# Kernel optimization log

Measured on AMD Instinct MI355X. Metric: run time of the kernel, lower is better.

Reference implementation:

```python
import jax, jax.numpy as jnp
import numpy as np

D_MODEL = 1024
SCALE = float(np.sqrt(D_MODEL))


def setup_inputs() -> dict:
    key = jax.random.key(0)
    k1, k2, k3 = jax.random.split(key, 3)
    input_data = jax.random.normal(k1, (4, 2048, D_MODEL), dtype=jnp.float32)
    qk = jax.random.normal(k2, (D_MODEL, D_MODEL), dtype=jnp.float32) / SCALE
    ov = jax.random.normal(k3, (D_MODEL, D_MODEL), dtype=jnp.float32) / SCALE
    return {"input_data": input_data, "qk": qk, "ov": ov}


def reference(input_data, qk, ov):
    # input_data: [B, S, D]; qk, ov: [D, D]
    S = input_data.shape[1]
    # scores: [B, S, S] = (x @ qk) @ x^T / sqrt(D)
    scores = jnp.einsum("bsd,de,bte->bst", input_data, qk, input_data) / SCALE
    # causal mask: positions t > s get -inf (upper triangle, diagonal=1)
    causal = jnp.tril(jnp.ones((S, S), dtype=bool))
    scores = jnp.where(causal, scores, -jnp.inf)
    attn = jax.nn.softmax(scores, axis=-1)
    # A: [B, S, D] = attn @ x @ ov
    return jnp.einsum("bst,btd,de->bse", attn, input_data, ov)
```

## Files before the change

### kernel.cpp

```cpp
#include <hip/hip_runtime.h>
#include <hip/hip_bf16.h>
#include <cstdint>
#include <cstddef>
#include <type_traits>


using bf16 = __hip_bfloat16;
typedef __attribute__((ext_vector_type(8))) short short8;
typedef __attribute__((ext_vector_type(4))) float f32x4;

#define NB 4
#define SS 2048
#define DD 1024

__device__ __forceinline__ void async_lds16(const bf16* g, bf16* l) {
  __builtin_amdgcn_global_load_lds(
      (const __attribute__((address_space(1))) void*)g,
      (__attribute__((address_space(3))) void*)l,
      16, 0, 0);
}

struct alignas(8) bf16x4s { bf16 a, b, c, d; };

__global__ __launch_bounds__(256) void prep_kernel(const float* __restrict__ x,
                                                   bf16* __restrict__ xb,
                                                   const float* __restrict__ qk,
                                                   bf16* __restrict__ qkT,
                                                   const float* __restrict__ ov,
                                                   bf16* __restrict__ ovT,
                                                   float* __restrict__ l) {
  __shared__ bf16 tile[64][65];
  const int bx = blockIdx.x;
  if (bx < 8192) {
    int i = (bx * 256 + threadIdx.x) * 4;
    float4 v = *(const float4*)(x + i);
    bf16x4s o{__float2bfloat16(v.x), __float2bfloat16(v.y),
              __float2bfloat16(v.z), __float2bfloat16(v.w)};
    *(bf16x4s*)(xb + i) = o;
  } else if (bx < 8704) {
    const int idx = bx - 8192;
    const float* in = (idx & 256) ? ov : qk;
    bf16* out = (idx & 256) ? ovT : qkT;
    const int rem = idx & 255;
    const int tbx = (rem & 15) * 64;
    const int tby = (rem >> 4) * 64;
    const int tc = threadIdx.x & 63;
    const int tr = threadIdx.x >> 6;
#pragma unroll
    for (int r = tr; r < 64; r += 4)
      tile[tc][r] = __float2bfloat16(in[(size_t)(tby + r) * DD + tbx + tc]);
    __syncthreads();
#pragma unroll
    for (int r = tr; r < 64; r += 4)
      out[(size_t)(tbx + r) * DD + tby + tc] = tile[r][tc];
  } else {
    const int t = (bx - 8704) * 256 + threadIdx.x;
    f32x4 z = {0.f, 0.f, 0.f, 0.f};
    *(f32x4*)(l + t * 4) = z;
  }
}

__device__ __forceinline__ void gemm256_core(const bf16* __restrict__ Ab,
                                             const bf16* __restrict__ Bb,
                                             bf16* __restrict__ C,
                                             int N, int K, int m0, int n0, int nk,
                                             bf16* As, bf16* Bs) {
  const int lane = threadIdx.x & 63;
  const int wave = threadIdx.x >> 6;
  const int wr   = wave >> 2;
  const int wc   = wave & 3;
  const int quad = lane >> 4;
  const int r    = lane & 15;

  f32x4 acc[8][4];
#pragma unroll
  for (int i = 0; i < 8; ++i)
#pragma unroll
    for (int n = 0; n < 4; ++n) acc[i][n] = f32x4{0.f, 0.f, 0.f, 0.f};

  const int lrow = lane >> 3;
  const int lsw  = (lane & 7) ^ lrow;
  const long long a_lane = (long long)(m0 + wave * 8 + lrow) * K + lsw * 8;
  const long long b_lane = (long long)(n0 + wave * 8 + lrow) * K + lsw * 8;

  auto stageA = [&](int kt, int rnd, int buf) {
    async_lds16(Ab + a_lane + (long long)(rnd * 64) * K + (long long)kt * 64,
                As + buf * 16384 + (rnd * 64 + wave * 8) * 64);
  };
  auto stageB = [&](int kt, int rnd, int buf) {
    async_lds16(Bb + b_lane + (long long)(rnd * 64) * K + (long long)kt * 64,
                Bs + buf * 16384 + (rnd * 64 + wave * 8) * 64);
  };

  stageA(0, 0, 0); stageA(0, 2, 0);
  stageB(0, 0, 0); stageB(0, 1, 0); stageB(0, 2, 0); stageB(0, 3, 0);
  stageA(0, 1, 0); stageA(0, 3, 0);
  asm volatile("s_waitcnt vmcnt(2)" ::: "memory");
  asm volatile("s_barrier" ::: "memory");

  const int ca0 = (quad ^ (r & 7)) * 8;
  const int ca1 = ((4 + quad) ^ (r & 7)) * 8;

  for (int kt = 0; kt < nk; ++kt) {
    const int buf = kt & 1, nxt = buf ^ 1;
    const bool hn = (kt + 1 < nk);
    const bf16* Abuf = As + buf * 16384 + (wr * 128) * 64;
    const bf16* Bbuf = Bs + buf * 16384 + (wc * 64) * 64;

    auto phase = [&](auto RHC, int ca, auto&& stg, int wmode) {
      constexpr int RH = decltype(RHC)::value;
      short8 af[4], bfr[4];
#pragma unroll
      for (int m = 0; m < 4; ++m)
        af[m] = *(const short8*)(Abuf + (RH * 64 + m * 16 + r) * 64 + ca);
#pragma unroll
      for (int n = 0; n < 4; ++n)
        bfr[n] = *(const short8*)(Bbuf + (n * 16 + r) * 64 + ca);
      stg();
      asm volatile("s_barrier" ::: "memory");
      asm volatile("s_waitcnt lgkmcnt(0)" ::: "memory");
      __builtin_amdgcn_sched_barrier(0);
      __builtin_amdgcn_s_setprio(1);
#pragma unroll
      for (int m = 0; m < 4; ++m)
#pragma unroll
        for (int n = 0; n < 4; ++n)
          acc[RH * 4 + m][n] = __builtin_amdgcn_mfma_f32_16x16x32_bf16(
              af[m], bfr[n], acc[RH * 4 + m][n], 0, 0, 0);
      __builtin_amdgcn_s_setprio(0);
      if (wmode == 1) {
        if (hn) asm volatile("s_waitcnt vmcnt(2)" ::: "memory");
        else    asm volatile("s_waitcnt vmcnt(0)" ::: "memory");
      } else if (wmode == 2) {
        if (hn) asm volatile("s_waitcnt vmcnt(2)" ::: "memory");
      }
      asm volatile("s_barrier" ::: "memory");
    };

    phase(std::integral_constant<int, 0>{}, ca0,
          [&] { if (hn) { stageA(kt + 1, 0, nxt); stageA(kt + 1, 2, nxt); } }, 1);
    phase(std::integral_constant<int, 1>{}, ca0,
          [&] { if (hn) { stageB(kt + 1, 0, nxt); stageB(kt + 1, 1, nxt); } }, 0);
    phase(std::integral_constant<int, 0>{}, ca1,
          [&] { if (hn) { stageB(kt + 1, 2, nxt); stageB(kt + 1, 3, nxt); } }, 0);
    phase(std::integral_constant<int, 1>{}, ca1,
          [&] { if (hn) { stageA(kt + 1, 1, nxt); stageA(kt + 1, 3, nxt); } }, 2);
  }

#pragma unroll
  for (int i = 0; i < 8; ++i) {
    const int row0 = m0 + wr * 128 + i * 16 + quad * 4;
#pragma unroll
    for (int n = 0; n < 4; ++n) {
      const int col = n0 + wc * 64 + n * 16 + r;
#pragma unroll
      for (int q = 0; q < 4; ++q)
        C[(long long)(row0 + q) * N + col] = __float2bfloat16(acc[i][n][q]);
    }
  }
}

template <int EPI>
__device__ __forceinline__ void gemm128_core(const bf16* __restrict__ Ab,
                                             const bf16* __restrict__ Bb,
                                             void* __restrict__ C,
                                             float* __restrict__ l,
                                             int N, int K, int m0, int n0, int nk,
                                             bf16* As, bf16* Bs) {
  const int lane = threadIdx.x & 63;
  const int wave = threadIdx.x >> 6;
  const int wr   = wave >> 1;
  const int wc   = wave & 1;
  const int quad = lane >> 4;
  const int r    = lane & 15;

  f32x4 acc[4][4];
#pragma unroll
  for (int m = 0; m < 4; ++m)
#pragma unroll
    for (int n = 0; n < 4; ++n) acc[m][n] = f32x4{0.f, 0.f, 0.f, 0.f};

  const int lrow = lane >> 3;
  const int lsw  = (lane & 7) ^ lrow;
  const long long a_base = (long long)(m0 + wave * 32 + lrow) * K + lsw * 8;
  const long long b_base = (long long)(n0 + wave * 32 + lrow) * K + lsw * 8;

  auto stageA = [&](int kt, int buf) {
#pragma unroll
    for (int i = 0; i < 4; ++i)
      async_lds16(Ab + a_base + (long long)(i * 8) * K + (long long)kt * 64,
                  As + buf * 8192 + (wave * 32 + i * 8) * 64);
  };
  auto stageB = [&](int kt, int buf) {
#pragma unroll
    for (int i = 0; i < 4; ++i)
      async_lds16(Bb + b_base + (long long)(i * 8) * K + (long long)kt * 64,
                  Bs + buf * 8192 + (wave * 32 + i * 8) * 64);
  };

  stageB(0, 0); stageA(0, 0); stageA(1, 1);
  asm volatile("s_waitcnt vmcnt(4)" ::: "memory");
  asm volatile("s_barrier" ::: "memory");

  const int ca0 = (quad ^ (r & 7)) * 8;
  const int ca1 = ((4 + quad) ^ (r & 7)) * 8;

  int ba = 0;
  for (int kt = 0; kt < nk; ++kt) {
    const int bb = kt & 1;
    int ba2 = ba + 2; if (ba2 >= 3) ba2 -= 3;
    const bool hA = (kt + 2 < nk), hB = (kt + 1 < nk);
    const bf16* Abuf = As + ba * 8192;
    const bf16* Bbuf = Bs + bb * 8192;

    auto phase = [&](int ca, auto&& stg, bool tail) {
      short8 af[4], bfr[4];
#pragma unroll
      for (int m = 0; m < 4; ++m)
        af[m] = *(const short8*)(Abuf + (wr * 64 + m * 16 + r) * 64 + ca);
#pragma unroll
      for (int n = 0; n < 4; ++n)
        bfr[n] = *(const short8*)(Bbuf + (wc * 64 + n * 16 + r) * 64 + ca);
      stg();
      asm volatile("s_barrier" ::: "memory");
      asm volatile("s_waitcnt lgkmcnt(0)" ::: "memory");
      __builtin_amdgcn_sched_barrier(0);
      __builtin_amdgcn_s_setprio(1);
#pragma unroll
      for (int m = 0; m < 4; ++m)
#pragma unroll
        for (int n = 0; n < 4; ++n)
          acc[m][n] = __builtin_amdgcn_mfma_f32_16x16x32_bf16(
              af[m], bfr[n], acc[m][n], 0, 0, 0);
      __builtin_amdgcn_s_setprio(0);
      if (tail) {
        if (hA)      asm volatile("s_waitcnt vmcnt(4)" ::: "memory");
        else if (hB) asm volatile("s_waitcnt vmcnt(0)" ::: "memory");
      }
      asm volatile("s_barrier" ::: "memory");
    };

    phase(ca0, [&] { if (hB) stageB(kt + 1, bb ^ 1);
                     if (hA) stageA(kt + 2, ba2); }, false);
    phase(ca1, [&] {}, true);

    if (++ba == 3) ba = 0;
  }

#pragma unroll
  for (int m = 0; m < 4; ++m) {
    const int row0 = m0 + wr * 64 + m * 16 + quad * 4;
    if (EPI == 2) {
      float qs[4] = {0.f, 0.f, 0.f, 0.f};
#pragma unroll
      for (int n = 0; n < 4; ++n) {
        const int col = n0 + wc * 64 + n * 16 + r;
#pragma unroll
        for (int q = 0; q < 4; ++q) {
          const int row = row0 + q;
          float v = (col <= row) ? __expf(acc[m][n][q] * 0.03125f) : 0.0f;
          ((bf16*)C)[(long long)row * N + col] = __float2bfloat16(v);
          qs[q] += v;
        }
      }
#pragma unroll
      for (int q = 0; q < 4; ++q) {
#pragma unroll
        for (int off = 1; off < 16; off <<= 1) qs[q] += __shfl_xor(qs[q], off, 64);
        if (r == 0) atomicAdd(&l[row0 + q], qs[q]);
      }
    } else {
      float rs[4];
#pragma unroll
      for (int q = 0; q < 4; ++q) rs[q] = 1.0f / l[row0 + q];
#pragma unroll
      for (int n = 0; n < 4; ++n) {
        const int col = n0 + wc * 64 + n * 16 + r;
#pragma unroll
        for (int q = 0; q < 4; ++q)
          ((float*)C)[(long long)(row0 + q) * N + col] = acc[m][n][q] * rs[q];
      }
    }
  }
}

__global__ __launch_bounds__(512, 2) void gemm_qv256(const bf16* __restrict__ xb,
                                                     const bf16* __restrict__ qkT,
                                                     const bf16* __restrict__ ovT,
                                                     bf16* __restrict__ Qb,
                                                     bf16* __restrict__ Vt) {
  extern __shared__ bf16 lds[];
  bf16* As = lds;
  bf16* Bs = lds + 32768;
  const long long SD = (long long)SS * DD;
  const int z = blockIdx.z;
  if (z < 4) {
    const int bn = blockIdx.x & 3, bm = blockIdx.x >> 2;
    gemm256_core(xb + z * SD, qkT, Qb + z * SD, DD, DD, bm * 256, bn * 256, 16, As, Bs);
  } else {
    const int bm = blockIdx.x & 3, bn = blockIdx.x >> 2;
    gemm256_core(ovT, xb + (z - 4) * SD, Vt + (z - 4) * SD, SS, DD, bm * 256, bn * 256, 16, As, Bs);
  }
}

__global__ __launch_bounds__(256, 2) void gemm_sc128(const bf16* __restrict__ Qb,
                                                     const bf16* __restrict__ xb,
                                                     bf16* __restrict__ P,
                                                     float* __restrict__ l) {
  extern __shared__ bf16 lds[];
  bf16* As = lds;
  bf16* Bs = lds + 24576;
  const long long SD = (long long)SS * DD;
  const long long SSQ = (long long)SS * SS;
  const int t = blockIdx.x;
  int bm = (int)((sqrtf(8.0f * (float)t + 1.0f) - 1.0f) * 0.5f);
  while ((bm + 1) * (bm + 2) / 2 <= t) ++bm;
  while (bm * (bm + 1) / 2 > t) --bm;
  const int bn = t - bm * (bm + 1) / 2;
  const int b = blockIdx.z;
  gemm128_core<2>(Qb + b * SD, xb + b * SD, P + b * SSQ, l + b * SS,
                  SS, DD, bm * 128, bn * 128, 16, As, Bs);
}

__global__ __launch_bounds__(256, 2) void gemm_pv128(const bf16* __restrict__ P,
                                                     const bf16* __restrict__ Vt,
                                                     float* __restrict__ l,
                                                     float* __restrict__ out) {
  extern __shared__ bf16 lds[];
  bf16* As = lds;
  bf16* Bs = lds + 24576;
  const long long SD = (long long)SS * DD;
  const long long SSQ = (long long)SS * SS;
  const int c  = blockIdx.x & 7;
  const int pr = blockIdx.x >> 3;
  const int b  = blockIdx.z;
  const int n0 = c * 128;
  const int rL = 15 - pr;
  gemm128_core<3>(P + b * SSQ, Vt + b * SD, out + b * SD, l + b * SS,
                  DD, SS, rL * 128, n0, 2 * (rL + 1), As, Bs);
  __syncthreads();
  gemm128_core<3>(P + b * SSQ, Vt + b * SD, out + b * SD, l + b * SS,
                  DD, SS, pr * 128, n0, 2 * (pr + 1), As, Bs);
}

extern "C" void kernel_launch(void* const* d_in, const int* in_sizes, int n_in,
                              void* d_out, int out_size, void* d_ws, size_t ws_size,
                              hipStream_t stream) {
  const float* x  = (const float*)d_in[0];
  const float* qk = (const float*)d_in[1];
  const float* ov = (const float*)d_in[2];
  float* out = (float*)d_out;

  char* ws = (char*)d_ws;
  const size_t MB = 1ull << 20;
  bf16*  xb  = (bf16*)(ws + 0);
  bf16*  qkT = (bf16*)(ws + 16 * MB);
  bf16*  ovT = (bf16*)(ws + 18 * MB);
  bf16*  Qb  = (bf16*)(ws + 20 * MB);
  bf16*  Vt  = (bf16*)(ws + 36 * MB);
  bf16*  P   = (bf16*)(ws + 52 * MB);
  float* l   = (float*)(ws + 84 * MB);

  static bool lds_opt_in = false;
  if (!lds_opt_in) {
    hipFuncSetAttribute((const void*)gemm_qv256,
                        hipFuncAttributeMaxDynamicSharedMemorySize, 131072);
    hipFuncSetAttribute((const void*)gemm_sc128,
                        hipFuncAttributeMaxDynamicSharedMemorySize, 81920);
    hipFuncSetAttribute((const void*)gemm_pv128,
                        hipFuncAttributeMaxDynamicSharedMemorySize, 81920);
    lds_opt_in = true;
  }

  prep_kernel<<<dim3(8712), 256, 0, stream>>>(x, xb, qk, qkT, ov, ovT, l);
  gemm_qv256<<<dim3(32, 1, 8), 512, 131072, stream>>>(xb, qkT, ovT, Qb, Vt);
  gemm_sc128<<<dim3(136, 1, 4), 256, 81920, stream>>>(Qb, xb, P, l);
  gemm_pv128<<<dim3(64, 1, 4), 256, 81920, stream>>>(P, Vt, l, out);
}
```

Baseline: 199.0 us.

## Use BK=32 K-tiles with a 4-stage unified LDS pipeline in gemm128_core

The 128x128 GEMM core goes from 64-wide K tiles (3 A buffers, 2 B buffers, two half-phases per tile) to 32-wide K tiles held in a 4-deep ring shared by A and B, prefetching three tiles ahead. The swizzle, load mapping and waitcnt accounting are rewritten to match, and the dynamic LDS request drops from 80KB to 64KB. The intent is deeper memory latency hiding and a simpler schedule with less LDS. In exchange each iteration does half the MFMA work per barrier pair, so sync overhead per FLOP roughly doubles.

New measurement: 201.4 us. Within noise of the previous version (+1.2%).

```diff
diff --git a/kernel.cpp b/kernel.cpp
--- a/kernel.cpp
+++ b/kernel.cpp
@@ -180,71 +180,65 @@
 #pragma unroll
     for (int n = 0; n < 4; ++n) acc[m][n] = f32x4{0.f, 0.f, 0.f, 0.f};
 
-  const int lrow = lane >> 3;
-  const int lsw  = (lane & 7) ^ lrow;
+  const int lrow = lane >> 2;
+  const int lsw  = (lane & 3) ^ (lrow & 3);
   const long long a_base = (long long)(m0 + wave * 32 + lrow) * K + lsw * 8;
   const long long b_base = (long long)(n0 + wave * 32 + lrow) * K + lsw * 8;
 
   auto stageA = [&](int kt, int buf) {
 #pragma unroll
-    for (int i = 0; i < 4; ++i)
-      async_lds16(Ab + a_base + (long long)(i * 8) * K + (long long)kt * 64,
-                  As + buf * 8192 + (wave * 32 + i * 8) * 64);
+    for (int i = 0; i < 2; ++i)
+      async_lds16(Ab + a_base + (long long)(i * 16) * K + (long long)kt * 32,
+                  As + buf * 4096 + (wave * 32 + i * 16) * 32);
   };
   auto stageB = [&](int kt, int buf) {
 #pragma unroll
-    for (int i = 0; i < 4; ++i)
-      async_lds16(Bb + b_base + (long long)(i * 8) * K + (long long)kt * 64,
-                  Bs + buf * 8192 + (wave * 32 + i * 8) * 64);
+    for (int i = 0; i < 2; ++i)
+      async_lds16(Bb + b_base + (long long)(i * 16) * K + (long long)kt * 32,
+                  Bs + buf * 4096 + (wave * 32 + i * 16) * 32);
   };
 
-  stageB(0, 0); stageA(0, 0); stageA(1, 1);
-  asm volatile("s_waitcnt vmcnt(4)" ::: "memory");
+  stageB(0, 0); stageA(0, 0);
+  if (nk > 1) { stageB(1, 1); stageA(1, 1); }
+  if (nk > 2) { stageB(2, 2); stageA(2, 2); }
+  if (nk > 2)      asm volatile("s_waitcnt vmcnt(8)" ::: "memory");
+  else if (nk > 1) asm volatile("s_waitcnt vmcnt(4)" ::: "memory");
+  else             asm volatile("s_waitcnt vmcnt(0)" ::: "memory");
   asm volatile("s_barrier" ::: "memory");
 
-  const int ca0 = (quad ^ (r & 7)) * 8;
-  const int ca1 = ((4 + quad) ^ (r & 7)) * 8;
-
-  int ba = 0;
-  for (int kt = 0; kt < nk; ++kt) {
-    const int bb = kt & 1;
-    int ba2 = ba + 2; if (ba2 >= 3) ba2 -= 3;
-    const bool hA = (kt + 2 < nk), hB = (kt + 1 < nk);
-    const bf16* Abuf = As + ba * 8192;
-    const bf16* Bbuf = Bs + bb * 8192;
-
-    auto phase = [&](int ca, auto&& stg, bool tail) {
-      short8 af[4], bfr[4];
-#pragma unroll
-      for (int m = 0; m < 4; ++m)
-        af[m] = *(const short8*)(Abuf + (wr * 64 + m * 16 + r) * 64 + ca);
+  const int ca = (quad ^ (r & 3)) * 8;
+
+  for (int t = 0; t < nk; ++t) {
+    const int bt = t & 3, b3 = (t + 3) & 3;
+    const bf16* Abuf = As + bt * 4096;
+    const bf16* Bbuf = Bs + bt * 4096;
+
+    short8 af[4], bfr[4];
+#pragma unroll
+    for (int m = 0; m < 4; ++m)
+      af[m] = *(const short8*)(Abuf + (wr * 64 + m * 16 + r) * 32 + ca);
+#pragma unroll
+    for (int n = 0; n < 4; ++n)
+      bfr[n] = *(const short8*)(Bbuf + (wc * 64 + n * 16 + r) * 32 + ca);
+
+    if (t + 3 < nk) { stageB(t + 3, b3); stageA(t + 3, b3); }
+
+    asm volatile("s_barrier" ::: "memory");
+    asm volatile("s_waitcnt lgkmcnt(0)" ::: "memory");
+    __builtin_amdgcn_sched_barrier(0);
+    __builtin_amdgcn_s_setprio(1);
+#pragma unroll
+    for (int m = 0; m < 4; ++m)
 #pragma unroll
       for (int n = 0; n < 4; ++n)
-        bfr[n] = *(const short8*)(Bbuf + (wc * 64 + n * 16 + r) * 64 + ca);
-      stg();
-      asm volatile("s_barrier" ::: "memory");
-      asm volatile("s_waitcnt lgkmcnt(0)" ::: "memory");
-      __builtin_amdgcn_sched_barrier(0);
-      __builtin_amdgcn_s_setprio(1);
-#pragma unroll
-      for (int m = 0; m < 4; ++m)
-#pragma unroll
-        for (int n = 0; n < 4; ++n)
-          acc[m][n] = __builtin_amdgcn_mfma_f32_16x16x32_bf16(
-              af[m], bfr[n], acc[m][n], 0, 0, 0);
-      __builtin_amdgcn_s_setprio(0);
-      if (tail) {
-        if (hA)      asm volatile("s_waitcnt vmcnt(4)" ::: "memory");
-        else if (hB) asm volatile("s_waitcnt vmcnt(0)" ::: "memory");
-      }
-      asm volatile("s_barrier" ::: "memory");
-    };
-
-    phase(ca0, [&] { if (hB) stageB(kt + 1, bb ^ 1);
-                     if (hA) stageA(kt + 2, ba2); }, false);
-    phase(ca1, [&] {}, true);
-
-    if (++ba == 3) ba = 0;
+        acc[m][n] = __builtin_amdgcn_mfma_f32_16x16x32_bf16(
+            af[m], bfr[n], acc[m][n], 0, 0, 0);
+    __builtin_amdgcn_s_setprio(0);
+
+    if (t + 3 < nk)      asm volatile("s_waitcnt vmcnt(8)" ::: "memory");
+    else if (t + 2 < nk) asm volatile("s_waitcnt vmcnt(4)" ::: "memory");
+    else if (t + 1 < nk) asm volatile("s_waitcnt vmcnt(0)" ::: "memory");
+    asm volatile("s_barrier" ::: "memory");
   }
 
 #pragma unroll
@@ -309,7 +303,7 @@
                                                      float* __restrict__ l) {
   extern __shared__ bf16 lds[];
   bf16* As = lds;
-  bf16* Bs = lds + 24576;
+  bf16* Bs = lds + 16384;
   const long long SD = (long long)SS * DD;
   const long long SSQ = (long long)SS * SS;
   const int t = blockIdx.x;
@@ -319,7 +313,7 @@
   const int bn = t - bm * (bm + 1) / 2;
   const int b = blockIdx.z;
   gemm128_core<2>(Qb + b * SD, xb + b * SD, P + b * SSQ, l + b * SS,
-                  SS, DD, bm * 128, bn * 128, 16, As, Bs);
+                  SS, DD, bm * 128, bn * 128, 32, As, Bs);
 }
 
 __global__ __launch_bounds__(256, 2) void gemm_pv128(const bf16* __restrict__ P,
@@ -328,7 +322,7 @@
                                                      float* __restrict__ out) {
   extern __shared__ bf16 lds[];
   bf16* As = lds;
-  bf16* Bs = lds + 24576;
+  bf16* Bs = lds + 16384;
   const long long SD = (long long)SS * DD;
   const long long SSQ = (long long)SS * SS;
   const int c  = blockIdx.x & 7;
@@ -337,10 +331,10 @@
   const int n0 = c * 128;
   const int rL = 15 - pr;
   gemm128_core<3>(P + b * SSQ, Vt + b * SD, out + b * SD, l + b * SS,
-                  DD, SS, rL * 128, n0, 2 * (rL + 1), As, Bs);
+                  DD, SS, rL * 128, n0, 4 * (rL + 1), As, Bs);
   __syncthreads();
   gemm128_core<3>(P + b * SSQ, Vt + b * SD, out + b * SD, l + b * SS,
-                  DD, SS, pr * 128, n0, 2 * (pr + 1), As, Bs);
+                  DD, SS, pr * 128, n0, 4 * (pr + 1), As, Bs);
 }
 
 extern "C" void kernel_launch(void* const* d_in, const int* in_sizes, int n_in,
@@ -366,14 +360,14 @@
     hipFuncSetAttribute((const void*)gemm_qv256,
                         hipFuncAttributeMaxDynamicSharedMemorySize, 131072);
     hipFuncSetAttribute((const void*)gemm_sc128,
-                        hipFuncAttributeMaxDynamicSharedMemorySize, 81920);
+                        hipFuncAttributeMaxDynamicSharedMemorySize, 65536);
     hipFuncSetAttribute((const void*)gemm_pv128,
-                        hipFuncAttributeMaxDynamicSharedMemorySize, 81920);
+                        hipFuncAttributeMaxDynamicSharedMemorySize, 65536);
     lds_opt_in = true;
   }
 
   prep_kernel<<<dim3(8712), 256, 0, stream>>>(x, xb, qk, qkT, ov, ovT, l);
   gemm_qv256<<<dim3(32, 1, 8), 512, 131072, stream>>>(xb, qkT, ovT, Qb, Vt);
-  gemm_sc128<<<dim3(136, 1, 4), 256, 81920, stream>>>(Qb, xb, P, l);
-  gemm_pv128<<<dim3(64, 1, 4), 256, 81920, stream>>>(P, Vt, l, out);
-}
+  gemm_sc128<<<dim3(136, 1, 4), 256, 65536, stream>>>(Qb, xb, P, l);
+  gemm_pv128<<<dim3(64, 1, 4), 256, 65536, stream>>>(P, Vt, l, out);
+}
```

## Use 64x128 tiles for causal score GEMM with finer triangular block mapping

Applied to the files above, without the earlier changes.

Replaces the 128x128 score GEMM with a dedicated 64x128 tile kernel that uses double-buffered LDS, a smaller LDS footprint and three blocks per CU. A new block-index mapping enumerates 64-row strips against 128-column tiles of the causal triangle, so fewer fully masked tiles are computed and more blocks are available to fill the GPU. In exchange each block reuses less data from its loads, and the pipeline is simpler than the original three-stage A buffering.

After: 191.8 us, median of 3. -3.6%, faster.

```diff
diff --git a/kernel.cpp b/kernel.cpp
--- a/kernel.cpp
+++ b/kernel.cpp
@@ -160,13 +160,113 @@
   }
 }
 
-template <int EPI>
-__device__ __forceinline__ void gemm128_core(const bf16* __restrict__ Ab,
-                                             const bf16* __restrict__ Bb,
-                                             void* __restrict__ C,
-                                             float* __restrict__ l,
-                                             int N, int K, int m0, int n0, int nk,
-                                             bf16* As, bf16* Bs) {
+__device__ __forceinline__ void gemm64_sc(const bf16* __restrict__ Ab,
+                                          const bf16* __restrict__ Bb,
+                                          bf16* __restrict__ P,
+                                          float* __restrict__ l,
+                                          int N, int K, int m0, int n0, int nk,
+                                          bf16* As, bf16* Bs) {
+  const int lane = threadIdx.x & 63;
+  const int wave = threadIdx.x >> 6;
+  const int wm   = (wave >> 1) * 32;
+  const int wn   = (wave & 1) * 64;
+  const int quad = lane >> 4;
+  const int r    = lane & 15;
+
+  f32x4 acc[2][4];
+#pragma unroll
+  for (int m = 0; m < 2; ++m)
+#pragma unroll
+    for (int n = 0; n < 4; ++n) acc[m][n] = f32x4{0.f, 0.f, 0.f, 0.f};
+
+  const int lrow = lane >> 3;
+  const int lsw  = (lane & 7) ^ lrow;
+  const long long a_lane = (long long)(m0 + lrow) * K + lsw * 8;
+  const long long b_lane = (long long)(n0 + lrow) * K + lsw * 8;
+
+  auto stageA = [&](int kt, int rnd, int buf) {
+    async_lds16(Ab + a_lane + (long long)(rnd * 32 + wave * 8) * K + (long long)kt * 64,
+                As + buf * 4096 + (rnd * 32 + wave * 8) * 64);
+  };
+  auto stageB = [&](int kt, int rnd, int buf) {
+    async_lds16(Bb + b_lane + (long long)(rnd * 32 + wave * 8) * K + (long long)kt * 64,
+                Bs + buf * 8192 + (rnd * 32 + wave * 8) * 64);
+  };
+
+  stageA(0, 0, 0); stageA(0, 1, 0);
+  stageB(0, 0, 0); stageB(0, 1, 0); stageB(0, 2, 0); stageB(0, 3, 0);
+  asm volatile("s_waitcnt vmcnt(0)" ::: "memory");
+  asm volatile("s_barrier" ::: "memory");
+
+  const int ca0 = (quad ^ (r & 7)) * 8;
+  const int ca1 = ((4 + quad) ^ (r & 7)) * 8;
+
+  for (int kt = 0; kt < nk; ++kt) {
+    const int buf = kt & 1, nxt = buf ^ 1;
+    const bool hn = (kt + 1 < nk);
+    const bf16* Abuf = As + buf * 4096;
+    const bf16* Bbuf = Bs + buf * 8192;
+
+    auto phase = [&](int ca, auto&& stg, bool tail) {
+      short8 af[2], bfr[4];
+#pragma unroll
+      for (int m = 0; m < 2; ++m)
+        af[m] = *(const short8*)(Abuf + (wm + m * 16 + r) * 64 + ca);
+#pragma unroll
+      for (int n = 0; n < 4; ++n)
+        bfr[n] = *(const short8*)(Bbuf + (wn + n * 16 + r) * 64 + ca);
+      stg();
+      asm volatile("s_barrier" ::: "memory");
+      asm volatile("s_waitcnt lgkmcnt(0)" ::: "memory");
+      __builtin_amdgcn_sched_barrier(0);
+      __builtin_amdgcn_s_setprio(1);
+#pragma unroll
+      for (int m = 0; m < 2; ++m)
+#pragma unroll
+        for (int n = 0; n < 4; ++n)
+          acc[m][n] = __builtin_amdgcn_mfma_f32_16x16x32_bf16(
+              af[m], bfr[n], acc[m][n], 0, 0, 0);
+      __builtin_amdgcn_s_setprio(0);
+      if (tail && hn) asm volatile("s_waitcnt vmcnt(0)" ::: "memory");
+      asm volatile("s_barrier" ::: "memory");
+    };
+
+    phase(ca0, [&] { if (hn) { stageA(kt + 1, 0, nxt); stageA(kt + 1, 1, nxt);
+                               stageB(kt + 1, 0, nxt); } }, false);
+    phase(ca1, [&] { if (hn) { stageB(kt + 1, 1, nxt); stageB(kt + 1, 2, nxt);
+                               stageB(kt + 1, 3, nxt); } }, true);
+  }
+
+#pragma unroll
+  for (int m = 0; m < 2; ++m) {
+    const int row0 = m0 + wm + m * 16 + quad * 4;
+    float qs[4] = {0.f, 0.f, 0.f, 0.f};
+#pragma unroll
+    for (int n = 0; n < 4; ++n) {
+      const int col = n0 + wn + n * 16 + r;
+#pragma unroll
+      for (int q = 0; q < 4; ++q) {
+        const int row = row0 + q;
+        float v = (col <= row) ? __expf(acc[m][n][q] * 0.03125f) : 0.0f;
+        P[(long long)row * N + col] = __float2bfloat16(v);
+        qs[q] += v;
+      }
+    }
+#pragma unroll
+    for (int q = 0; q < 4; ++q) {
+#pragma unroll
+      for (int off = 1; off < 16; off <<= 1) qs[q] += __shfl_xor(qs[q], off, 64);
+      if (r == 0) atomicAdd(&l[row0 + q], qs[q]);
+    }
+  }
+}
+
+__device__ __forceinline__ void gemm128_pv(const bf16* __restrict__ Ab,
+                                           const bf16* __restrict__ Bb,
+                                           float* __restrict__ C,
+                                           const float* __restrict__ l,
+                                           int N, int K, int m0, int n0, int nk,
+                                           bf16* As, bf16* Bs) {
   const int lane = threadIdx.x & 63;
   const int wave = threadIdx.x >> 6;
   const int wr   = wave >> 1;
@@ -250,36 +350,15 @@
 #pragma unroll
   for (int m = 0; m < 4; ++m) {
     const int row0 = m0 + wr * 64 + m * 16 + quad * 4;
-    if (EPI == 2) {
-      float qs[4] = {0.f, 0.f, 0.f, 0.f};
-#pragma unroll
-      for (int n = 0; n < 4; ++n) {
-        const int col = n0 + wc * 64 + n * 16 + r;
-#pragma unroll
-        for (int q = 0; q < 4; ++q) {
-          const int row = row0 + q;
-          float v = (col <= row) ? __expf(acc[m][n][q] * 0.03125f) : 0.0f;
-          ((bf16*)C)[(long long)row * N + col] = __float2bfloat16(v);
-          qs[q] += v;
-        }
-      }
-#pragma unroll
-      for (int q = 0; q < 4; ++q) {
-#pragma unroll
-        for (int off = 1; off < 16; off <<= 1) qs[q] += __shfl_xor(qs[q], off, 64);
-        if (r == 0) atomicAdd(&l[row0 + q], qs[q]);
-      }
-    } else {
-      float rs[4];
-#pragma unroll
-      for (int q = 0; q < 4; ++q) rs[q] = 1.0f / l[row0 + q];
-#pragma unroll
-      for (int n = 0; n < 4; ++n) {
-        const int col = n0 + wc * 64 + n * 16 + r;
-#pragma unroll
-        for (int q = 0; q < 4; ++q)
-          ((float*)C)[(long long)(row0 + q) * N + col] = acc[m][n][q] * rs[q];
-      }
+    float rs[4];
+#pragma unroll
+    for (int q = 0; q < 4; ++q) rs[q] = 1.0f / l[row0 + q];
+#pragma unroll
+    for (int n = 0; n < 4; ++n) {
+      const int col = n0 + wc * 64 + n * 16 + r;
+#pragma unroll
+      for (int q = 0; q < 4; ++q)
+        C[(long long)(row0 + q) * N + col] = acc[m][n][q] * rs[q];
     }
   }
 }
@@ -303,23 +382,25 @@
   }
 }
 
-__global__ __launch_bounds__(256, 2) void gemm_sc128(const bf16* __restrict__ Qb,
-                                                     const bf16* __restrict__ xb,
-                                                     bf16* __restrict__ P,
-                                                     float* __restrict__ l) {
+__global__ __launch_bounds__(256, 3) void gemm_sc64(const bf16* __restrict__ Qb,
+                                                    const bf16* __restrict__ xb,
+                                                    bf16* __restrict__ P,
+                                                    float* __restrict__ l) {
   extern __shared__ bf16 lds[];
   bf16* As = lds;
-  bf16* Bs = lds + 24576;
+  bf16* Bs = lds + 8192;
   const long long SD = (long long)SS * DD;
   const long long SSQ = (long long)SS * SS;
   const int t = blockIdx.x;
-  int bm = (int)((sqrtf(8.0f * (float)t + 1.0f) - 1.0f) * 0.5f);
-  while ((bm + 1) * (bm + 2) / 2 <= t) ++bm;
-  while (bm * (bm + 1) / 2 > t) --bm;
-  const int bn = t - bm * (bm + 1) / 2;
+  int k = (int)((sqrtf(4.0f * (float)t + 1.0f) - 1.0f) * 0.5f);
+  while ((k + 1) * (k + 2) <= t) ++k;
+  while (k * (k + 1) > t) --k;
+  int s, c;
+  if (t < (k + 1) * (k + 1)) { s = 2 * k;     c = t - k * (k + 1); }
+  else                       { s = 2 * k + 1; c = t - (k + 1) * (k + 1); }
   const int b = blockIdx.z;
-  gemm128_core<2>(Qb + b * SD, xb + b * SD, P + b * SSQ, l + b * SS,
-                  SS, DD, bm * 128, bn * 128, 16, As, Bs);
+  gemm64_sc(Qb + b * SD, xb + b * SD, P + b * SSQ, l + b * SS,
+            SS, DD, s * 64, c * 128, 16, As, Bs);
 }
 
 __global__ __launch_bounds__(256, 2) void gemm_pv128(const bf16* __restrict__ P,
@@ -336,11 +417,11 @@
   const int b  = blockIdx.z;
   const int n0 = c * 128;
   const int rL = 15 - pr;
-  gemm128_core<3>(P + b * SSQ, Vt + b * SD, out + b * SD, l + b * SS,
-                  DD, SS, rL * 128, n0, 2 * (rL + 1), As, Bs);
+  gemm128_pv(P + b * SSQ, Vt + b * SD, out + b * SD, l + b * SS,
+             DD, SS, rL * 128, n0, 2 * (rL + 1), As, Bs);
   __syncthreads();
-  gemm128_core<3>(P + b * SSQ, Vt + b * SD, out + b * SD, l + b * SS,
-                  DD, SS, pr * 128, n0, 2 * (pr + 1), As, Bs);
+  gemm128_pv(P + b * SSQ, Vt + b * SD, out + b * SD, l + b * SS,
+             DD, SS, pr * 128, n0, 2 * (pr + 1), As, Bs);
 }
 
 extern "C" void kernel_launch(void* const* d_in, const int* in_sizes, int n_in,
@@ -365,8 +446,8 @@
   if (!lds_opt_in) {
     hipFuncSetAttribute((const void*)gemm_qv256,
                         hipFuncAttributeMaxDynamicSharedMemorySize, 131072);
-    hipFuncSetAttribute((const void*)gemm_sc128,
-                        hipFuncAttributeMaxDynamicSharedMemorySize, 81920);
+    hipFuncSetAttribute((const void*)gemm_sc64,
+                        hipFuncAttributeMaxDynamicSharedMemorySize, 49152);
     hipFuncSetAttribute((const void*)gemm_pv128,
                         hipFuncAttributeMaxDynamicSharedMemorySize, 81920);
     lds_opt_in = true;
@@ -374,6 +455,6 @@
 
   prep_kernel<<<dim3(8712), 256, 0, stream>>>(x, xb, qk, qkT, ov, ovT, l);
   gemm_qv256<<<dim3(32, 1, 8), 512, 131072, stream>>>(xb, qkT, ovT, Qb, Vt);
-  gemm_sc128<<<dim3(136, 1, 4), 256, 81920, stream>>>(Qb, xb, P, l);
+  gemm_sc64<<<dim3(272, 1, 4), 256, 49152, stream>>>(Qb, xb, P, l);
   gemm_pv128<<<dim3(64, 1, 4), 256, 81920, stream>>>(P, Vt, l, out);
 }
```
